# Performance work log

Measured on AMD Instinct MI355X. Metric: run time of the kernel, lower is better.

The kernel has to match this reference:

```python
import jax, jax.numpy as jnp
import numpy as np

DIM = 1024
HEADS = 16


def setup_inputs() -> dict:
    key = jax.random.key(0)
    ks = jax.random.split(key, 9)
    B, N, C = 2, 2048, DIM
    hd = C // HEADS
    s = 1.0 / np.sqrt(C)
    x = jax.random.normal(ks[0], (B, N, C), dtype=jnp.float32)
    wq = jax.random.normal(ks[1], (C, C), dtype=jnp.float32) * s
    wk = jax.random.normal(ks[2], (C, C), dtype=jnp.float32) * s
    wv = jax.random.normal(ks[3], (C, C), dtype=jnp.float32) * s
    wp = jax.random.normal(ks[4], (C, C), dtype=jnp.float32) * s
    bp = jnp.zeros((C,), dtype=jnp.float32)
    # rotary table: angles theta_j = 10000^{-2j/hd}, positions 0..N-1
    inv_freq = 1.0 / (10000.0 ** (jnp.arange(0, hd, 2, dtype=jnp.float32) / hd))
    ang = jnp.arange(N, dtype=jnp.float32)[:, None] * inv_freq[None, :]  # (N, hd//2)
    cos = jnp.cos(ang)
    sin = jnp.sin(ang)
    return {"x": x, "wq": wq, "wk": wk, "wv": wv, "wp": wp, "bp": bp,
            "cos": cos, "sin": sin, "num_heads": HEADS}


def _apply_rotary(t, cos, sin):
    # t: (B, N, H, D); cos/sin: (N, D//2) -> broadcast (1, N, 1, D//2)
    B, N, H, D = t.shape
    tr = t.reshape(B, N, H, D // 2, 2)
    t1, t2 = tr[..., 0], tr[..., 1]
    c = cos[None, :, None, :]
    s = sin[None, :, None, :]
    o1 = t1 * c - t2 * s
    o2 = t1 * s + t2 * c
    return jnp.stack([o1, o2], axis=-1).reshape(B, N, H, D)


def reference(x, wq, wk, wv, wp, bp, cos, sin, num_heads):
    B, N, C = x.shape
    H = num_heads
    D = C // H
    q = (x @ wq.T).reshape(B, N, H, D)
    k = (x @ wk.T).reshape(B, N, H, D)
    v = (x @ wv.T).reshape(B, N, H, D)
    q = _apply_rotary(q, cos, sin)
    k = _apply_rotary(k, cos, sin)
    scale = 1.0 / jnp.sqrt(jnp.asarray(D, dtype=x.dtype))
    # scores: (B, H, N, N)
    scores = jnp.einsum('bnhd,bmhd->bhnm', q, k) * scale
    attn = jax.nn.softmax(scores, axis=-1)
    out = jnp.einsum('bhnm,bmhd->bnhd', attn, v).reshape(B, N, C)
    return out @ wp.T + bp
```

## Files before the change

### kernel.cpp

```cpp
#include <hip/hip_runtime.h>
#include <hip/hip_bf16.h>
#include <stdint.h>

#define DEVI __device__ __forceinline__

using bf16 = __hip_bfloat16;
typedef __bf16 bf16x8 __attribute__((ext_vector_type(8)));
typedef __bf16 bf16x4 __attribute__((ext_vector_type(4)));
typedef float f32x4 __attribute__((ext_vector_type(4)));

static constexpr int Bb = 2, Nn = 2048, Cc = 1024, Hh = 16, Dd = 64;
static constexpr float CSC = 0.125f * 1.44269504088896340736f;

DEVI bf16 f2bf(float x) {
  __bf16 h = (__bf16)x;
  return *(bf16*)&h;
}
DEVI float fexp2(float x) { return __builtin_amdgcn_exp2f(x); }

DEVI bf16x8 cvt8(f32x4 a, f32x4 b) {
  bf16x8 r;
  r[0] = (__bf16)a[0]; r[1] = (__bf16)a[1]; r[2] = (__bf16)a[2]; r[3] = (__bf16)a[3];
  r[4] = (__bf16)b[0]; r[5] = (__bf16)b[1]; r[6] = (__bf16)b[2]; r[7] = (__bf16)b[3];
  return r;
}

DEVI void gld_lds16(const bf16* g, bf16* l) {
  __builtin_amdgcn_global_load_lds(
      (__attribute__((address_space(1))) void*)(g),
      (__attribute__((address_space(3))) void*)(l),
      16, 0, 0);
}

__global__ __launch_bounds__(256) void k_cvt(const float* __restrict__ x,
                                             const float* __restrict__ wq,
                                             const float* __restrict__ wk,
                                             const float* __restrict__ wv,
                                             const float* __restrict__ wp,
                                             bf16* xb, bf16* wqb, bf16* wkb,
                                             bf16* wvb, bf16* wpb) {
  int bid = blockIdx.x;
  const float* src; bf16* dst; size_t off;
  if (bid < 2048) {
    src = x; dst = xb; off = (size_t)bid * 2048;
  } else {
    int s = (bid - 2048) >> 9, r = (bid - 2048) & 511;
    off = (size_t)r * 2048;
    src = s == 0 ? wq : s == 1 ? wk : s == 2 ? wv : wp;
    dst = s == 0 ? wqb : s == 1 ? wkb : s == 2 ? wvb : wpb;
  }
  size_t i = off + (size_t)threadIdx.x * 8;
  f32x4 a = *(const f32x4*)(src + i);
  f32x4 b = *(const f32x4*)(src + i + 4);
  *(bf16x8*)(dst + i) = cvt8(a, b);
}

template <int MFC, class Epi>
DEVI void gemm_dbuf(const bf16* __restrict__ A, const bf16* __restrict__ Bw,
                    int K, int m0, int n0, bf16* lA, bf16* lB, Epi epi) {
  constexpr int BM = MFC * 32;
  constexpr int PA = BM / 64;
  constexpr int ASZ = BM * 32, BSZ = 128 * 32;
  const int t = threadIdx.x;
  const int lane = t & 63, wave = t >> 6, g = lane >> 4;
  const int wr = wave >> 1, wc = wave & 1;

  auto stage = [&](int k0, int buf) {
#pragma unroll
    for (int p = 0; p < PA; ++p) {
      int c = p * 256 + t;
      gld_lds16(A + (size_t)(m0 + (c >> 2)) * K + k0 + (c & 3) * 8,
                lA + buf * ASZ + (size_t)(p * 256 + wave * 64) * 8);
    }
#pragma unroll
    for (int p = 0; p < 2; ++p) {
      int c = p * 256 + t;
      gld_lds16(Bw + (size_t)(n0 + (c >> 2)) * K + k0 + (c & 3) * 8,
                lB + buf * BSZ + (size_t)(p * 256 + wave * 64) * 8);
    }
  };

  f32x4 acc[MFC][4] = {};
  stage(0, 0);
  __syncthreads();

  const int NS = K / 32;
  for (int s = 0; s < NS; ++s) {
    const int cur = s & 1;
    if (s + 1 < NS) stage((s + 1) * 32, cur ^ 1);

    bf16x8 aF[MFC];
#pragma unroll
    for (int mf = 0; mf < MFC; ++mf)
      aF[mf] = *(const bf16x8*)(lA + cur * ASZ +
                                (wr * (BM / 2) + mf * 16 + (lane & 15)) * 32 + g * 8);
#pragma unroll
    for (int nf = 0; nf < 4; ++nf) {
      bf16x8 bF = *(const bf16x8*)(lB + cur * BSZ +
                                   (wc * 64 + nf * 16 + (lane & 15)) * 32 + g * 8);
#pragma unroll
      for (int mf = 0; mf < MFC; ++mf)
        acc[mf][nf] = __builtin_amdgcn_mfma_f32_16x16x32_bf16(aF[mf], bF, acc[mf][nf], 0, 0, 0);
    }
    __syncthreads();
  }

#pragma unroll
  for (int mf = 0; mf < MFC; ++mf)
#pragma unroll
    for (int nf = 0; nf < 4; ++nf)
#pragma unroll
      for (int r = 0; r < 4; ++r) {
        int gm = m0 + wr * (BM / 2) + mf * 16 + g * 4 + r;
        int gn = n0 + wc * 64 + nf * 16 + (lane & 15);
        epi(gm, gn, acc[mf][nf][r]);
      }
}

struct EpiRope {
  bf16* dst; const float* cosw; const float* sinw; float scale;
  DEVI void operator()(int gm, int gn, float v) const {
    int b = gm >> 11, n = gm & 2047;
    int h = gn >> 6, d = gn & 63;
    int i = d >> 1;
    float c = cosw[n * 32 + i], s = sinw[n * 32 + i];
    float p = __shfl_xor(v, 1);
    float o = (d & 1) ? (p * s + v * c) : (v * c - p * s);
    dst[((size_t)(b * Hh + h) * Nn + n) * 64 + d] = f2bf(o * scale);
  }
};

struct EpiVt {
  bf16* dst;
  DEVI void operator()(int gm, int gn, float v) const {
    int h = gm >> 6, d = gm & 63;
    int b = gn >> 11, n = gn & 2047;
    dst[((size_t)(b * Hh + h) * 64 + d) * Nn + n] = f2bf(v);
  }
};

struct EpiProj {
  float* dst; const float* bias;
  DEVI void operator()(int gm, int gn, float v) const {
    dst[(size_t)gm * Cc + gn] = v + bias[gn];
  }
};

__global__ __launch_bounds__(256) void k_qkv(const bf16* __restrict__ xb,
                                             const bf16* __restrict__ wqb,
                                             const bf16* __restrict__ wkb,
                                             const bf16* __restrict__ wvb,
                                             bf16* q_ws, bf16* k_ws, bf16* vt_ws,
                                             const float* __restrict__ cw,
                                             const float* __restrict__ sw) {
  __shared__ __align__(16) bf16 lA[2 * 128 * 32];
  __shared__ __align__(16) bf16 lB[2 * 128 * 32];
  int bid = blockIdx.x;
  if (bid < 512) {
    int sub = bid & 255;
    int m0 = (sub >> 3) * 128, n0 = (sub & 7) * 128;
    bool isq = bid < 256;
    gemm_dbuf<4>(xb, isq ? wqb : wkb, Cc, m0, n0, lA, lB,
                 EpiRope{isq ? q_ws : k_ws, cw, sw, isq ? CSC : 1.0f});
  } else {
    int sub = bid - 512;
    int m0 = (sub & 7) * 128, n0 = (sub >> 3) * 128;
    gemm_dbuf<4>(wvb, xb, Cc, m0, n0, lA, lB, EpiVt{vt_ws});
  }
}

__global__ __launch_bounds__(256) void k_proj(const bf16* __restrict__ A,
                                              const bf16* __restrict__ W,
                                              float* dst, const float* __restrict__ bias) {
  __shared__ __align__(16) bf16 lA[2 * 64 * 32];
  __shared__ __align__(16) bf16 lB[2 * 128 * 32];
  gemm_dbuf<2>(A, W, Cc, blockIdx.x * 64, blockIdx.y * 128, lA, lB,
               EpiProj{dst, bias});
}

__global__ __launch_bounds__(256) void k_flash(const bf16* __restrict__ q_ws,
                                               const bf16* __restrict__ k_ws,
                                               const bf16* __restrict__ vt_ws,
                                               bf16* __restrict__ attn_o) {
  __shared__ __align__(16) bf16 lK[2][64 * 64];
  __shared__ __align__(16) bf16 lV[2][64 * 64];
  __shared__ __align__(16) bf16 pbuf[4][32 * 64];

  const int t = threadIdx.x, lane = t & 63, wave = t >> 6;
  const int g = lane >> 4;
  const int bh = blockIdx.y;
  const int q0 = blockIdx.x * 128 + wave * 32;
  const bf16* qg = q_ws + (size_t)bh * Nn * 64;
  const bf16* kg = k_ws + (size_t)bh * Nn * 64;
  const bf16* vg = vt_ws + (size_t)bh * 64 * Nn;

  bf16x8 qF[2][2];
#pragma unroll
  for (int qs = 0; qs < 2; ++qs)
#pragma unroll
    for (int kd = 0; kd < 2; ++kd)
      qF[qs][kd] = *(const bf16x8*)(qg + (size_t)(q0 + qs * 16 + (lane & 15)) * 64 + kd * 32 + g * 8);

  f32x4 accO[2][4] = {};
  float LsL[2] = {0.f, 0.f};

  auto stage_tile = [&](int kt, int buf) {
#pragma unroll
    for (int p = 0; p < 2; ++p) {
      int c = p * 256 + t;
      int row = c >> 3, cis = (c & 7) ^ (row & 7);
      gld_lds16(kg + (size_t)(kt * 64 + row) * 64 + cis * 8,
                lK[buf] + (size_t)(p * 256 + wave * 64) * 8);
      gld_lds16(vg + (size_t)row * Nn + kt * 64 + cis * 8,
                lV[buf] + (size_t)(p * 256 + wave * 64) * 8);
    }
  };

  stage_tile(0, 0);
  __syncthreads();

  constexpr int NT = Nn / 64;
  for (int kt = 0; kt < NT; ++kt) {
    const int cur = kt & 1;
    if (kt + 1 < NT) stage_tile(kt + 1, cur ^ 1);

    f32x4 accT[2][4];
    __builtin_amdgcn_s_setprio(1);
#pragma unroll
    for (int nf = 0; nf < 4; ++nf) {
      int row = nf * 16 + (lane & 15);
      bf16x8 kF0 = *(const bf16x8*)(lK[cur] + ((row * 64 + 0 * 32 + g * 8) ^ ((row & 7) << 3)));
      bf16x8 kF1 = *(const bf16x8*)(lK[cur] + ((row * 64 + 1 * 32 + g * 8) ^ ((row & 7) << 3)));
#pragma unroll
      for (int qs = 0; qs < 2; ++qs) {
        f32x4 sacc = {};
        sacc = __builtin_amdgcn_mfma_f32_16x16x32_bf16(kF0, qF[qs][0], sacc, 0, 0, 0);
        sacc = __builtin_amdgcn_mfma_f32_16x16x32_bf16(kF1, qF[qs][1], sacc, 0, 0, 0);
        accT[qs][nf] = sacc;
      }
    }
    __builtin_amdgcn_s_setprio(0);

#pragma unroll
    for (int qs = 0; qs < 2; ++qs) {
      int prow = qs * 16 + (lane & 15);
      float ps = 0.f;
#pragma unroll
      for (int nf = 0; nf < 4; ++nf) {
        bf16x4 pk;
#pragma unroll
        for (int r = 0; r < 4; ++r) {
          float pv = fexp2(accT[qs][nf][r]);
          ps += pv;
          pk[r] = (__bf16)pv;
        }
        int idx = (prow * 64 + nf * 16 + g * 4) ^ ((prow & 7) << 3);
        *(bf16x4*)(pbuf[wave] + idx) = pk;
      }
      LsL[qs] += ps;
    }

    __builtin_amdgcn_s_setprio(1);
#pragma unroll
    for (int kd = 0; kd < 2; ++kd) {
      bf16x8 pF[2];
#pragma unroll
      for (int qs = 0; qs < 2; ++qs) {
        int prow = qs * 16 + (lane & 15);
        pF[qs] = *(const bf16x8*)(pbuf[wave] + ((prow * 64 + kd * 32 + g * 8) ^ ((prow & 7) << 3)));
      }
#pragma unroll
      for (int nf = 0; nf < 4; ++nf) {
        int row = nf * 16 + (lane & 15);
        bf16x8 vF = *(const bf16x8*)(lV[cur] + ((row * 64 + kd * 32 + g * 8) ^ ((row & 7) << 3)));
#pragma unroll
        for (int qs = 0; qs < 2; ++qs)
          accO[qs][nf] = __builtin_amdgcn_mfma_f32_16x16x32_bf16(pF[qs], vF, accO[qs][nf], 0, 0, 0);
      }
    }
    __builtin_amdgcn_s_setprio(0);

    __syncthreads();
  }

  float Lq[2];
#pragma unroll
  for (int qs = 0; qs < 2; ++qs) {
    float s = LsL[qs];
    s += __shfl_xor(s, 16);
    s += __shfl_xor(s, 32);
    Lq[qs] = s;
  }

  const int b = bh >> 4, h = bh & 15;
#pragma unroll
  for (int qs = 0; qs < 2; ++qs)
#pragma unroll
    for (int r = 0; r < 4; ++r) {
      float inv = 1.0f / __shfl(Lq[qs], g * 4 + r);
      int qrow = q0 + qs * 16 + g * 4 + r;
#pragma unroll
      for (int nf = 0; nf < 4; ++nf) {
        int d = nf * 16 + (lane & 15);
        attn_o[((size_t)(b * Nn + qrow)) * Cc + h * 64 + d] = f2bf(accO[qs][nf][r] * inv);
      }
    }
}

extern "C" void kernel_launch(void* const* d_in, const int* in_sizes, int n_in,
                              void* d_out, int out_size, void* d_ws, size_t ws_size,
                              hipStream_t stream) {
  (void)in_sizes; (void)n_in; (void)out_size; (void)ws_size;
  const float* x  = (const float*)d_in[0];
  const float* wq = (const float*)d_in[1];
  const float* wk = (const float*)d_in[2];
  const float* wv = (const float*)d_in[3];
  const float* wp = (const float*)d_in[4];
  const float* bp = (const float*)d_in[5];
  const float* cw = (const float*)d_in[6];
  const float* sw = (const float*)d_in[7];
  float* out = (float*)d_out;

  const size_t M1 = 1u << 20;
  bf16* x_bf  = (bf16*)d_ws;
  bf16* wq_bf = x_bf + 4 * M1;
  bf16* wk_bf = wq_bf + M1;
  bf16* wv_bf = wk_bf + M1;
  bf16* wp_bf = wv_bf + M1;
  bf16* q_ws  = wp_bf + M1;
  bf16* k_ws  = q_ws + 4 * M1;
  bf16* vt_ws = k_ws + 4 * M1;
  bf16* ao_ws = x_bf;

  k_cvt  <<<dim3(4096),    dim3(256), 0, stream>>>(x, wq, wk, wv, wp,
                                                   x_bf, wq_bf, wk_bf, wv_bf, wp_bf);
  k_qkv  <<<dim3(768),     dim3(256), 0, stream>>>(x_bf, wq_bf, wk_bf, wv_bf,
                                                   q_ws, k_ws, vt_ws, cw, sw);
  k_flash<<<dim3(16, 32),  dim3(256), 0, stream>>>(q_ws, k_ws, vt_ws, ao_ws);
  k_proj <<<dim3(64, 8),   dim3(256), 0, stream>>>(ao_ws, wp_bf, out, bp);
}
```

Measured before the change: 130.1 us.

## Switch flash attention to 32x32x16 MFMA with register-resident P via permlane32 swap

Rewrites the attention inner loop to use 32x32x16 bf16 MFMA tiles instead of 16x16x32. The softmax probabilities stay in registers and are rearranged into the B-operand layout with permlane32_swap, so the per-wave LDS P buffer and its write/read round trip go away. This cuts LDS traffic and shared memory per block, at the cost of a more intricate lane mapping and larger accumulator register use.

After: 132.6 us. No clear change (+1.9%).

```diff
diff --git a/kernel.cpp b/kernel.cpp
--- a/kernel.cpp
+++ b/kernel.cpp
@@ -8,6 +8,8 @@
 typedef __bf16 bf16x8 __attribute__((ext_vector_type(8)));
 typedef __bf16 bf16x4 __attribute__((ext_vector_type(4)));
 typedef float f32x4 __attribute__((ext_vector_type(4)));
+typedef float f32x16 __attribute__((ext_vector_type(16)));
+typedef int i32x2 __attribute__((ext_vector_type(2)));
 
 static constexpr int Bb = 2, Nn = 2048, Cc = 1024, Hh = 16, Dd = 64;
 static constexpr float CSC = 0.125f * 1.44269504088896340736f;
@@ -23,6 +25,18 @@
   r[0] = (__bf16)a[0]; r[1] = (__bf16)a[1]; r[2] = (__bf16)a[2]; r[3] = (__bf16)a[3];
   r[4] = (__bf16)b[0]; r[5] = (__bf16)b[1]; r[6] = (__bf16)b[2]; r[7] = (__bf16)b[3];
   return r;
+}
+
+DEVI uint32_t pk2(float a, float b) {
+  __bf16 x = (__bf16)a, y = (__bf16)b;
+  uint16_t ux = *(uint16_t*)&x, uy = *(uint16_t*)&y;
+  return (uint32_t)ux | ((uint32_t)uy << 16);
+}
+
+DEVI bf16x8 mk8(uint32_t a, uint32_t b, uint32_t c, uint32_t d) {
+  union { uint32_t u[4]; bf16x8 v; } x;
+  x.u[0] = a; x.u[1] = b; x.u[2] = c; x.u[3] = d;
+  return x.v;
 }
 
 DEVI void gld_lds16(const bf16* g, bf16* l) {
@@ -184,25 +198,22 @@
                                                bf16* __restrict__ attn_o) {
   __shared__ __align__(16) bf16 lK[2][64 * 64];
   __shared__ __align__(16) bf16 lV[2][64 * 64];
-  __shared__ __align__(16) bf16 pbuf[4][32 * 64];
 
   const int t = threadIdx.x, lane = t & 63, wave = t >> 6;
-  const int g = lane >> 4;
+  const int l31 = lane & 31, hi = lane >> 5;
   const int bh = blockIdx.y;
-  const int q0 = blockIdx.x * 128 + wave * 32;
+  const int q0w = blockIdx.x * 128 + wave * 32;
   const bf16* qg = q_ws + (size_t)bh * Nn * 64;
   const bf16* kg = k_ws + (size_t)bh * Nn * 64;
   const bf16* vg = vt_ws + (size_t)bh * 64 * Nn;
 
-  bf16x8 qF[2][2];
-#pragma unroll
-  for (int qs = 0; qs < 2; ++qs)
-#pragma unroll
-    for (int kd = 0; kd < 2; ++kd)
-      qF[qs][kd] = *(const bf16x8*)(qg + (size_t)(q0 + qs * 16 + (lane & 15)) * 64 + kd * 32 + g * 8);
-
-  f32x4 accO[2][4] = {};
-  float LsL[2] = {0.f, 0.f};
+  bf16x8 qF[4];
+#pragma unroll
+  for (int kd = 0; kd < 4; ++kd)
+    qF[kd] = *(const bf16x8*)(qg + (size_t)(q0w + l31) * 64 + kd * 16 + hi * 8);
+
+  f32x16 accO[2] = {};
+  float LsL = 0.f;
 
   auto stage_tile = [&](int kt, int buf) {
 #pragma unroll
@@ -224,87 +235,65 @@
     const int cur = kt & 1;
     if (kt + 1 < NT) stage_tile(kt + 1, cur ^ 1);
 
-    f32x4 accT[2][4];
-    __builtin_amdgcn_s_setprio(1);
-#pragma unroll
-    for (int nf = 0; nf < 4; ++nf) {
-      int row = nf * 16 + (lane & 15);
-      bf16x8 kF0 = *(const bf16x8*)(lK[cur] + ((row * 64 + 0 * 32 + g * 8) ^ ((row & 7) << 3)));
-      bf16x8 kF1 = *(const bf16x8*)(lK[cur] + ((row * 64 + 1 * 32 + g * 8) ^ ((row & 7) << 3)));
-#pragma unroll
-      for (int qs = 0; qs < 2; ++qs) {
-        f32x4 sacc = {};
-        sacc = __builtin_amdgcn_mfma_f32_16x16x32_bf16(kF0, qF[qs][0], sacc, 0, 0, 0);
-        sacc = __builtin_amdgcn_mfma_f32_16x16x32_bf16(kF1, qF[qs][1], sacc, 0, 0, 0);
-        accT[qs][nf] = sacc;
+#pragma unroll
+    for (int kb = 0; kb < 2; ++kb) {
+      f32x16 accT = {};
+      __builtin_amdgcn_s_setprio(1);
+#pragma unroll
+      for (int kd = 0; kd < 4; ++kd) {
+        int row = kb * 32 + l31;
+        bf16x8 kF = *(const bf16x8*)(lK[cur] +
+            ((row * 64 + kd * 16 + hi * 8) ^ ((row & 7) << 3)));
+        accT = __builtin_amdgcn_mfma_f32_32x32x16_bf16(kF, qF[kd], accT, 0, 0, 0);
       }
-    }
-    __builtin_amdgcn_s_setprio(0);
-
-#pragma unroll
-    for (int qs = 0; qs < 2; ++qs) {
-      int prow = qs * 16 + (lane & 15);
-      float ps = 0.f;
-#pragma unroll
-      for (int nf = 0; nf < 4; ++nf) {
-        bf16x4 pk;
-#pragma unroll
-        for (int r = 0; r < 4; ++r) {
-          float pv = fexp2(accT[qs][nf][r]);
-          ps += pv;
-          pk[r] = (__bf16)pv;
+      __builtin_amdgcn_s_setprio(0);
+
+      float p[16];
+#pragma unroll
+      for (int r = 0; r < 16; ++r) { p[r] = fexp2(accT[r]); LsL += p[r]; }
+
+      uint32_t c01 = pk2(p[0], p[1]),  c23 = pk2(p[2], p[3]);
+      uint32_t c89 = pk2(p[4], p[5]),  cab = pk2(p[6], p[7]);
+      uint32_t d01 = pk2(p[8], p[9]),  d23 = pk2(p[10], p[11]);
+      uint32_t d89 = pk2(p[12], p[13]), dab = pk2(p[14], p[15]);
+      i32x2 s0a = __builtin_amdgcn_permlane32_swap((int)c01, (int)c89, false, false);
+      i32x2 s0b = __builtin_amdgcn_permlane32_swap((int)c23, (int)cab, false, false);
+      i32x2 s1a = __builtin_amdgcn_permlane32_swap((int)d01, (int)d89, false, false);
+      i32x2 s1b = __builtin_amdgcn_permlane32_swap((int)d23, (int)dab, false, false);
+      bf16x8 paF[2] = { mk8(s0a[0], s0b[0], s0a[1], s0b[1]),
+                        mk8(s1a[0], s1b[0], s1a[1], s1b[1]) };
+
+      __builtin_amdgcn_s_setprio(1);
+#pragma unroll
+      for (int d0 = 0; d0 < 2; ++d0) {
+#pragma unroll
+        for (int s = 0; s < 2; ++s) {
+          int vrow = d0 * 32 + l31;
+          bf16x8 vF = *(const bf16x8*)(lV[cur] +
+              ((vrow * 64 + kb * 32 + s * 16 + hi * 8) ^ ((vrow & 7) << 3)));
+          accO[d0] = __builtin_amdgcn_mfma_f32_32x32x16_bf16(paF[s], vF, accO[d0], 0, 0, 0);
         }
-        int idx = (prow * 64 + nf * 16 + g * 4) ^ ((prow & 7) << 3);
-        *(bf16x4*)(pbuf[wave] + idx) = pk;
       }
-      LsL[qs] += ps;
-    }
-
-    __builtin_amdgcn_s_setprio(1);
-#pragma unroll
-    for (int kd = 0; kd < 2; ++kd) {
-      bf16x8 pF[2];
-#pragma unroll
-      for (int qs = 0; qs < 2; ++qs) {
-        int prow = qs * 16 + (lane & 15);
-        pF[qs] = *(const bf16x8*)(pbuf[wave] + ((prow * 64 + kd * 32 + g * 8) ^ ((prow & 7) << 3)));
-      }
-#pragma unroll
-      for (int nf = 0; nf < 4; ++nf) {
-        int row = nf * 16 + (lane & 15);
-        bf16x8 vF = *(const bf16x8*)(lV[cur] + ((row * 64 + kd * 32 + g * 8) ^ ((row & 7) << 3)));
-#pragma unroll
-        for (int qs = 0; qs < 2; ++qs)
-          accO[qs][nf] = __builtin_amdgcn_mfma_f32_16x16x32_bf16(pF[qs], vF, accO[qs][nf], 0, 0, 0);
-      }
-    }
-    __builtin_amdgcn_s_setprio(0);
+      __builtin_amdgcn_s_setprio(0);
+    }
 
     __syncthreads();
   }
 
-  float Lq[2];
-#pragma unroll
-  for (int qs = 0; qs < 2; ++qs) {
-    float s = LsL[qs];
-    s += __shfl_xor(s, 16);
-    s += __shfl_xor(s, 32);
-    Lq[qs] = s;
-  }
+  float L = LsL + __shfl_xor(LsL, 32);
 
   const int b = bh >> 4, h = bh & 15;
 #pragma unroll
-  for (int qs = 0; qs < 2; ++qs)
-#pragma unroll
-    for (int r = 0; r < 4; ++r) {
-      float inv = 1.0f / __shfl(Lq[qs], g * 4 + r);
-      int qrow = q0 + qs * 16 + g * 4 + r;
-#pragma unroll
-      for (int nf = 0; nf < 4; ++nf) {
-        int d = nf * 16 + (lane & 15);
-        attn_o[((size_t)(b * Nn + qrow)) * Cc + h * 64 + d] = f2bf(accO[qs][nf][r] * inv);
-      }
-    }
+  for (int r = 0; r < 16; ++r) {
+    int ql = (r & 3) + 8 * (r >> 2) + 4 * hi;
+    float inv = 1.0f / __shfl(L, ql);
+    int qrow = q0w + ql;
+#pragma unroll
+    for (int d0 = 0; d0 < 2; ++d0) {
+      int d = d0 * 32 + l31;
+      attn_o[((size_t)(b * Nn + qrow)) * Cc + h * 64 + d] = f2bf(accO[d0][r] * inv);
+    }
+  }
 }
 
 extern "C" void kernel_launch(void* const* d_in, const int* in_sizes, int n_in,
```
